# Kernel tuning notes

Hardware: AMD Instinct MI355X
Metric: run time of the kernel (lower is better)

Reference implementation:

```python
import jax, jax.numpy as jnp
import numpy as np

K = 3  # kernel size


def _bilinear_sample(x, px, py):
    """Bilinear sample x:[b,c,h,w] at pixel coords px,py:[b,t,h,w].
    Zeros padding, align_corners=True semantics (coords are raw pixel coords).
    Returns [b,c,t,h,w]."""
    b, c, h, w = x.shape
    x0 = jnp.floor(px)
    y0 = jnp.floor(py)
    wx1 = px - x0
    wx0 = 1.0 - wx1
    wy1 = py - y0
    wy0 = 1.0 - wy1
    xf = x.reshape(b, c, h * w)

    def gather(xi, yi):
        valid = (xi >= 0) & (xi <= w - 1) & (yi >= 0) & (yi <= h - 1)
        xi_c = jnp.clip(xi, 0, w - 1).astype(jnp.int32)
        yi_c = jnp.clip(yi, 0, h - 1).astype(jnp.int32)
        idx = (yi_c * w + xi_c).reshape(b, 1, -1)  # [b,1,t*h*w]
        v = jnp.take_along_axis(xf, idx, axis=2).reshape(b, c, *xi.shape[1:])
        return v * valid[:, None].astype(x.dtype)

    out = (gather(x0, y0) * (wx0 * wy0)[:, None]
           + gather(x0 + 1, y0) * (wx1 * wy0)[:, None]
           + gather(x0, y0 + 1) * (wx0 * wy1)[:, None]
           + gather(x0 + 1, y0 + 1) * (wx1 * wy1)[:, None])
    return out


def setup_inputs() -> dict:
    key = jax.random.key(0)
    k1, k2, k3 = jax.random.split(key, 3)
    b, c, h, w = 4, 64, 128, 128
    out_c = 64
    x = jax.random.normal(k1, (b, c, h, w), dtype=jnp.float32)
    offset = jax.random.normal(k2, (b, 2 * K * K, h, w), dtype=jnp.float32)
    weight = jax.random.normal(k3, (out_c, c, K, K), dtype=jnp.float32) * 0.05
    bias = jnp.zeros((out_c,), dtype=jnp.float32)
    return {"x": x, "offset": offset, "weight": weight, "bias": bias}


def reference(x, offset, weight, bias):
    b, c, h, w = x.shape
    kk = K * K
    # base integer grid (x along width, y along height)
    yy, xx = jnp.meshgrid(jnp.arange(h, dtype=x.dtype), jnp.arange(w, dtype=x.dtype), indexing='ij')
    off = offset.reshape(b, kk, 2, h, w)
    # grid_sample with align_corners=True inverts the module's normalization,
    # so effective sampling coords are simply base + offset in pixel space.
    px = xx[None, None] + off[:, :, 0]  # [b,kk,h,w]
    py = yy[None, None] + off[:, :, 1]
    sampled = _bilinear_sample(x, px, py)  # [b,c,kk,h,w]
    w2 = weight.reshape(weight.shape[0], c, kk)  # [o,c,kk]
    out = jnp.einsum('oct,bcthw->bohw', w2, sampled)
    return out + bias[None, :, None, None]
```

## Files before the change

### kernel.cpp

```cpp
#include <hip/hip_runtime.h>
#include <cstddef>

#define BH 4
#define CH 64
#define OH 64
#define HH 128
#define WW 128
#define KK 9
#define HW (HH * WW)

#define HX 4
#define HY 4
#define TW 25
#define TH 13
#define NREC (TW * TH)
#define NCHUNK (NREC * 8)

typedef __attribute__((ext_vector_type(8))) short short8;
typedef __attribute__((ext_vector_type(4))) float f32x4;
typedef __attribute__((ext_vector_type(2))) float f32x2;
typedef __attribute__((ext_vector_type(4))) unsigned int uint4v;
typedef __attribute__((ext_vector_type(4))) unsigned short ushort4v;

__device__ __forceinline__ unsigned short f2bf(float f) {
    unsigned u = __float_as_uint(f);
    u += 0x7fffu + ((u >> 16) & 1u);
    return (unsigned short)(u >> 16);
}
__device__ __forceinline__ f32x2 bf2x2(unsigned d) {
    f32x2 r;
    r.x = __uint_as_float(d << 16);
    r.y = __uint_as_float(d & 0xffff0000u);
    return r;
}
__device__ __forceinline__ unsigned pack_bf2(f32x2 v) {
    unsigned u0 = __float_as_uint(v.x);
    u0 += 0x7fffu + ((u0 >> 16) & 1u);
    unsigned u1 = __float_as_uint(v.y);
    u1 += 0x7fffu + ((u1 >> 16) & 1u);
    return __builtin_amdgcn_perm(u1, u0, 0x07060302);
}
__device__ __forceinline__ uint4v combine4(uint4v c00, uint4v c10, uint4v c01, uint4v c11,
                                           float w00, float w10, float w01, float w11) {
    f32x2 W00 = {w00, w00}, W10 = {w10, w10}, W01 = {w01, w01}, W11 = {w11, w11};
    uint4v r;
#pragma unroll
    for (int j = 0; j < 4; ++j) {
        f32x2 s = W00 * bf2x2(c00[j]) + W10 * bf2x2(c10[j])
                + W01 * bf2x2(c01[j]) + W11 * bf2x2(c11[j]);
        r[j] = pack_bf2(s);
    }
    return r;
}

__global__ __launch_bounds__(256) void dcl_prep(const float* __restrict__ x,
                                                const float* __restrict__ wgt,
                                                unsigned short* __restrict__ xt,
                                                unsigned short* __restrict__ wtb) {
    if (blockIdx.x < 1024) {
        __shared__ float tile[64][65];
        int chunk = blockIdx.x;
        int b = chunk >> 8;
        int hw0 = (chunk & 255) * 64;
        int tid = threadIdx.x;
        int tx = tid & 63;
        int ty = tid >> 6;
        const float* xb = x + (size_t)b * CH * HW;
#pragma unroll
        for (int c = ty; c < 64; c += 4)
            tile[c][tx] = xb[(size_t)c * HW + hw0 + tx];
        __syncthreads();
        unsigned short* xtb = xt + ((size_t)b << 20);
        int c4 = (tid & 15) * 4;
        int p0 = tid >> 4;
#pragma unroll
        for (int it = 0; it < 4; ++it) {
            int pxl = p0 + it * 16;
            ushort4v v = { f2bf(tile[c4 + 0][pxl]), f2bf(tile[c4 + 1][pxl]),
                           f2bf(tile[c4 + 2][pxl]), f2bf(tile[c4 + 3][pxl]) };
            *(ushort4v*)(xtb + (size_t)(hw0 + pxl) * CH + c4) = v;
        }
    } else {
        int idx = (blockIdx.x - 1024) * 256 + threadIdx.x;
        int j  = idx & 7;
        int l  = (idx >> 3) & 63;
        int nt = (idx >> 9) & 3;
        int ks = idx >> 11;
        int k = ks * 32 + ((l >> 4) * 8) + j;
        int n = nt * 16 + (l & 15);
        int c = k & 63;
        int t = k >> 6;
        wtb[idx] = f2bf(wgt[(n * CH + c) * KK + t]);
    }
}

__global__ __launch_bounds__(256, 4) void dcl_main(
        const unsigned short* __restrict__ xt,
        const float* __restrict__ offset,
        const unsigned short* __restrict__ wtb,
        const float* __restrict__ bias,
        float* __restrict__ out) {
    __shared__ __align__(16) int smem[NREC * 32];
    int tid = threadIdx.x;
    int lane = tid & 63;
    int wave = tid >> 6;

    int b  = blockIdx.x >> 8;
    int t8 = blockIdx.x & 255;
    int x0 = (t8 & 7) << 4;
    int y0 = (t8 >> 3) << 2;
    int m = lane & 15;
    int quad = lane >> 4;
    int qoff = quad * 16;
    int y = y0 + wave;
    int pm = x0 + m;

    const char* xtb = (const char*)xt;
    const char* xim = xtb + (((size_t)b << 14) << 7);
    const float* ob = offset + (((size_t)(b * 18)) << 14) + (y << 7) + pm;
    float pxf = (float)pm;
    float pyf = (float)y;

    float oxv[9], oyv[9];
#pragma unroll
    for (int t = 0; t < 9; ++t) {
        oxv[t] = ob[(size_t)(2 * t) << 14];
        oyv[t] = ob[(size_t)(2 * t + 1) << 14];
    }

    uint4v* sv = (uint4v*)smem;
#pragma unroll
    for (int i = 0; i < 11; ++i) {
        int id = tid + i * 256;
        if (id < NCHUNK) {
            int p = id >> 3, sub = id & 7;
            int r = p / TW, col = p - r * TW;
            int sy = min(max(y0 - HY + r, 0), HH - 1);
            int sx = min(max(x0 - HX + col, 0), WW - 1);
            uint4v v = *(const uint4v*)(xim + (((sy << 7) + sx) << 7) + (sub << 4));
            sv[p * 8 + ((sub + (p & 7)) & 7)] = v;
        }
    }

    f32x4 acc[4];
#pragma unroll
    for (int i = 0; i < 4; ++i) acc[i] = (f32x4)(0.f);

    const short8* bfrags = (const short8*)wtb;

    __syncthreads();

#pragma unroll
    for (int t = 0; t < 9; ++t) {
        float fx = pxf + oxv[t];
        float fy = pyf + oyv[t];
        float x0f = floorf(fx), y0f = floorf(fy);
        float wx1 = fx - x0f, wy1 = fy - y0f;
        float wx0 = 1.0f - wx1, wy0 = 1.0f - wy1;
        int ix0 = (int)x0f, iy0 = (int)y0f;
        int ix1 = ix0 + 1, iy1 = iy0 + 1;
        bool vx0 = (unsigned)ix0 < (unsigned)WW;
        bool vx1 = (unsigned)ix1 < (unsigned)WW;
        bool vy0 = (unsigned)iy0 < (unsigned)HH;
        bool vy1 = (unsigned)iy1 < (unsigned)HH;
        float w00 = (vx0 && vy0) ? wx0 * wy0 : 0.0f;
        float w10 = (vx1 && vy0) ? wx1 * wy0 : 0.0f;
        float w01 = (vx0 && vy1) ? wx0 * wy1 : 0.0f;
        float w11 = (vx1 && vy1) ? wx1 * wy1 : 0.0f;
        int cx0 = min(max(ix0, 0), WW - 1), cx1 = min(max(ix1, 0), WW - 1);
        int cy0 = min(max(iy0, 0), HH - 1), cy1 = min(max(iy1, 0), HH - 1);

        int lc0 = cx0 - x0 + HX, lc1 = cx1 - x0 + HX;
        int lr0 = cy0 - y0 + HY, lr1 = cy1 - y0 + HY;
        bool oof = ((unsigned)lc0 > (TW - 1)) | ((unsigned)lc1 > (TW - 1)) |
                   ((unsigned)lr0 > (TH - 1)) | ((unsigned)lr1 > (TH - 1));
        int sc0 = min(max(lc0, 0), TW - 1), sc1 = min(max(lc1, 0), TW - 1);
        int sr0 = min(max(lr0, 0), TH - 1), sr1 = min(max(lr1, 0), TH - 1);
        int p00 = sr0 * TW + sc0, p10 = sr0 * TW + sc1;
        int p01 = sr1 * TW + sc0, p11 = sr1 * TW + sc1;

        uint4v c00a = sv[p00 * 8 + ((quad + (p00 & 7)) & 7)];
        uint4v c00b = sv[p00 * 8 + ((quad + 4 + (p00 & 7)) & 7)];
        uint4v c10a = sv[p10 * 8 + ((quad + (p10 & 7)) & 7)];
        uint4v c10b = sv[p10 * 8 + ((quad + 4 + (p10 & 7)) & 7)];
        uint4v c01a = sv[p01 * 8 + ((quad + (p01 & 7)) & 7)];
        uint4v c01b = sv[p01 * 8 + ((quad + 4 + (p01 & 7)) & 7)];
        uint4v c11a = sv[p11 * 8 + ((quad + (p11 & 7)) & 7)];
        uint4v c11b = sv[p11 * 8 + ((quad + 4 + (p11 & 7)) & 7)];

        if (__builtin_expect(oof, 0)) {
            int base = b << 14;
            int o00 = ((base + (cy0 << 7) + cx0) << 7) + qoff;
            int o10 = ((base + (cy0 << 7) + cx1) << 7) + qoff;
            int o01 = ((base + (cy1 << 7) + cx0) << 7) + qoff;
            int o11 = ((base + (cy1 << 7) + cx1) << 7) + qoff;
            c00a = *(const uint4v*)(xtb + o00);
            c00b = *(const uint4v*)(xtb + o00 + 64);
            c10a = *(const uint4v*)(xtb + o10);
            c10b = *(const uint4v*)(xtb + o10 + 64);
            c01a = *(const uint4v*)(xtb + o01);
            c01b = *(const uint4v*)(xtb + o01 + 64);
            c11a = *(const uint4v*)(xtb + o11);
            c11b = *(const uint4v*)(xtb + o11 + 64);
        }

        uint4v ra = combine4(c00a, c10a, c01a, c11a, w00, w10, w01, w11);
        uint4v rb = combine4(c00b, c10b, c01b, c11b, w00, w10, w01, w11);
        short8 aa = __builtin_bit_cast(short8, ra);
        short8 ab = __builtin_bit_cast(short8, rb);

        int ks = 2 * t;
#pragma unroll
        for (int nt = 0; nt < 4; ++nt)
            acc[nt] = __builtin_amdgcn_mfma_f32_16x16x32_bf16(
                aa, bfrags[(ks * 4 + nt) * 64 + lane], acc[nt], 0, 0, 0);
#pragma unroll
        for (int nt = 0; nt < 4; ++nt)
            acc[nt] = __builtin_amdgcn_mfma_f32_16x16x32_bf16(
                ab, bfrags[((ks + 1) * 4 + nt) * 64 + lane], acc[nt], 0, 0, 0);
    }

    __syncthreads();
    float* o_w = (float*)smem + wave * 1040;
#pragma unroll
    for (int nt = 0; nt < 4; ++nt)
#pragma unroll
        for (int reg = 0; reg < 4; ++reg)
            o_w[(quad * 4 + reg) * 65 + nt * 16 + m] = acc[nt][reg];
    __syncthreads();

    const float* os = (const float*)smem;
#pragma unroll
    for (int j = tid; j < 64 * 64; j += 256) {
        int o = j >> 6;
        int p = j & 63;
        int row = p >> 4, xx = p & 15;
        float v = os[row * 1040 + xx * 65 + o] + bias[o];
        out[(((size_t)(b * OH + o)) << 14) + ((y0 + row) << 7) + x0 + xx] = v;
    }
}

extern "C" void kernel_launch(void* const* d_in, const int* in_sizes, int n_in,
                              void* d_out, int out_size, void* d_ws, size_t ws_size,
                              hipStream_t stream) {
    const float* x      = (const float*)d_in[0];
    const float* offset = (const float*)d_in[1];
    const float* weight = (const float*)d_in[2];
    const float* bias   = (const float*)d_in[3];
    float* out = (float*)d_out;

    unsigned short* xt  = (unsigned short*)d_ws;
    unsigned short* wtb = (unsigned short*)((char*)d_ws + (size_t)BH * HW * CH * 2);

    dcl_prep<<<1024 + 144, 256, 0, stream>>>(x, weight, xt, wtb);
    dcl_main<<<(BH * HW) / 64, 256, 0, stream>>>(xt, offset, wtb, bias, out);
}
```

Measured before the change: 102.5 us.

## Shrink halo tile height and vectorize prep transpose loads and stores

Reduces the shared-memory halo tile from 13 to 12 rows, which cuts the per-block staging loads from 11 to 10 iterations and lowers shared-memory use. This risks more samples falling outside the tile and taking the slow global-memory fallback. The prep kernel's x-to-bf16 transpose now uses float4 global loads and 8-wide bf16 stores, with a padded tile row of 68, to reduce the number of memory transactions.

```diff
diff --git a/kernel.cpp b/kernel.cpp
--- a/kernel.cpp
+++ b/kernel.cpp
@@ -10,9 +10,9 @@
 #define HW (HH * WW)
 
 #define HX 4
-#define HY 4
+#define HYT 4
 #define TW 25
-#define TH 13
+#define TH 12
 #define NREC (TW * TH)
 #define NCHUNK (NREC * 8)
 
@@ -20,7 +20,7 @@
 typedef __attribute__((ext_vector_type(4))) float f32x4;
 typedef __attribute__((ext_vector_type(2))) float f32x2;
 typedef __attribute__((ext_vector_type(4))) unsigned int uint4v;
-typedef __attribute__((ext_vector_type(4))) unsigned short ushort4v;
+typedef __attribute__((ext_vector_type(8))) unsigned short ushort8v;
 
 __device__ __forceinline__ unsigned short f2bf(float f) {
     unsigned u = __float_as_uint(f);
@@ -58,27 +58,31 @@
                                                 unsigned short* __restrict__ xt,
                                                 unsigned short* __restrict__ wtb) {
     if (blockIdx.x < 1024) {
-        __shared__ float tile[64][65];
+        __shared__ float tile[64][68];
         int chunk = blockIdx.x;
         int b = chunk >> 8;
         int hw0 = (chunk & 255) * 64;
         int tid = threadIdx.x;
-        int tx = tid & 63;
-        int ty = tid >> 6;
-        const float* xb = x + (size_t)b * CH * HW;
-#pragma unroll
-        for (int c = ty; c < 64; c += 4)
-            tile[c][tx] = xb[(size_t)c * HW + hw0 + tx];
+        int cg = tid >> 4;
+        int tx4 = (tid & 15) * 4;
+        const float* xb = x + (size_t)b * CH * HW + hw0;
+#pragma unroll
+        for (int pass = 0; pass < 4; ++pass) {
+            int c = pass * 16 + cg;
+            float4 v = *(const float4*)(xb + (size_t)c * HW + tx4);
+            *(float4*)&tile[c][tx4] = v;
+        }
         __syncthreads();
-        unsigned short* xtb = xt + ((size_t)b << 20);
-        int c4 = (tid & 15) * 4;
-        int p0 = tid >> 4;
-#pragma unroll
-        for (int it = 0; it < 4; ++it) {
-            int pxl = p0 + it * 16;
-            ushort4v v = { f2bf(tile[c4 + 0][pxl]), f2bf(tile[c4 + 1][pxl]),
-                           f2bf(tile[c4 + 2][pxl]), f2bf(tile[c4 + 3][pxl]) };
-            *(ushort4v*)(xtb + (size_t)(hw0 + pxl) * CH + c4) = v;
+        unsigned short* xtb = xt + ((size_t)b << 20) + (size_t)hw0 * CH;
+        int c8 = (tid & 7) * 8;
+        int p0 = tid >> 3;
+#pragma unroll
+        for (int it = 0; it < 2; ++it) {
+            int pxl = p0 + it * 32;
+            ushort8v v;
+#pragma unroll
+            for (int j = 0; j < 8; ++j) v[j] = f2bf(tile[c8 + j][pxl]);
+            *(ushort8v*)(xtb + (size_t)pxl * CH + c8) = v;
         }
     } else {
         int idx = (blockIdx.x - 1024) * 256 + threadIdx.x;
@@ -130,12 +134,12 @@
 
     uint4v* sv = (uint4v*)smem;
 #pragma unroll
-    for (int i = 0; i < 11; ++i) {
+    for (int i = 0; i < 10; ++i) {
         int id = tid + i * 256;
         if (id < NCHUNK) {
             int p = id >> 3, sub = id & 7;
             int r = p / TW, col = p - r * TW;
-            int sy = min(max(y0 - HY + r, 0), HH - 1);
+            int sy = min(max(y0 - HYT + r, 0), HH - 1);
             int sx = min(max(x0 - HX + col, 0), WW - 1);
             uint4v v = *(const uint4v*)(xim + (((sy << 7) + sx) << 7) + (sub << 4));
             sv[p * 8 + ((sub + (p & 7)) & 7)] = v;
@@ -171,7 +175,7 @@
         int cy0 = min(max(iy0, 0), HH - 1), cy1 = min(max(iy1, 0), HH - 1);
 
         int lc0 = cx0 - x0 + HX, lc1 = cx1 - x0 + HX;
-        int lr0 = cy0 - y0 + HY, lr1 = cy1 - y0 + HY;
+        int lr0 = cy0 - y0 + HYT, lr1 = cy1 - y0 + HYT;
         bool oof = ((unsigned)lc0 > (TW - 1)) | ((unsigned)lc1 > (TW - 1)) |
                    ((unsigned)lr0 > (TH - 1)) | ((unsigned)lr1 > (TH - 1));
         int sc0 = min(max(lc0, 0), TW - 1), sc1 = min(max(lc1, 0), TW - 1);
```

Result: no change. 101.3 us (median of 2 runs) (-1.2%).
